# Optimization experiments

Hardware: AMD Instinct MI355X
Metric: run time of the kernel (lower is better)

## Reference

```python
import jax, jax.numpy as jnp
import numpy as np

B, S, D, H = 2, 2048, 1024, 16
DK = D // H  # 64

def setup_inputs() -> dict:
    key = jax.random.key(0)
    ks = jax.random.split(key, 12)
    scale = 1.0 / np.sqrt(D)
    return {
        "q": jax.random.normal(ks[0], (B, S, D), jnp.float32),
        "k": jax.random.normal(ks[1], (B, S, D), jnp.float32),
        "v": jax.random.normal(ks[2], (B, S, D), jnp.float32),
        "Wq": jax.random.normal(ks[3], (D, D), jnp.float32) * scale,
        "bq": jnp.zeros((D,), jnp.float32),
        "Wk": jax.random.normal(ks[4], (D, D), jnp.float32) * scale,
        "bk": jnp.zeros((D,), jnp.float32),
        "Wv": jax.random.normal(ks[5], (D, D), jnp.float32) * scale,
        "bv": jnp.zeros((D,), jnp.float32),
        "Wo": jax.random.normal(ks[6], (D, D), jnp.float32) * scale,
        "bo": jnp.zeros((D,), jnp.float32),
        "mask": jnp.ones((B, 1, S, S), jnp.bool_),
    }

def reference(q, k, v, Wq, bq, Wk, bk, Wv, bv, Wo, bo, mask):
    # Linear projections: y = x @ W^T + b (torch nn.Linear convention)
    def proj(x, W, b):
        return x @ W.T + b
    # [B,S,D] -> [B,H,S,DK]
    def split_heads(x):
        return x.reshape(B, S, H, DK).transpose(0, 2, 1, 3)

    query = split_heads(proj(q, Wq, bq))
    key_ = split_heads(proj(k, Wk, bk))
    value = split_heads(proj(v, Wv, bv))

    # NOTE: original uses out-of-place masked_fill whose result is discarded,
    # so mask has no effect on the computation (reproduced faithfully here).
    scores = jnp.einsum('bhqd,bhkd->bhqk', query, key_) / jnp.sqrt(
        jnp.asarray(DK, query.dtype))
    attn = jax.nn.softmax(scores, axis=-1)  # dropout p=0.0: identity
    x = jnp.einsum('bhqk,bhkd->bhqd', attn, value)
    x = x.transpose(0, 2, 1, 3).reshape(B, S, D)
    return proj(x, Wo, bo)
```

## Files before the change

kernel.cpp:

```cpp
#include <hip/hip_runtime.h>
#include <hip/hip_bf16.h>


typedef __attribute__((ext_vector_type(8))) short bf16x8;
typedef __attribute__((ext_vector_type(4))) float f32x4;
typedef unsigned short u16;
typedef unsigned int u32;

#define MFMA16(a, b, c) __builtin_amdgcn_mfma_f32_16x16x32_bf16(a, b, c, 0, 0, 0)
#define EXP2(x) __builtin_amdgcn_exp2f(x)

static __device__ __forceinline__ u16 f2bf(float f) {
    union { __hip_bfloat16 h; u16 u; } v;
    v.h = __float2bfloat16(f);
    return v.u;
}

static __device__ __forceinline__ u16 f2bf_fast(float f) {
    return (u16)((__float_as_uint(f) + 0x8000u) >> 16);
}

static __device__ __forceinline__ void gload16(const u16* g, u16* l) {
    __builtin_amdgcn_global_load_lds(
        (const __attribute__((address_space(1))) void*)g,
        (__attribute__((address_space(3))) void*)l, 16, 0, 0);
}

static __device__ __forceinline__ void cvt16(float4 f0, float4 f1,
                                             float4 f2, float4 f3, u16* o) {
    o[0]=f2bf(f0.x);  o[1]=f2bf(f0.y);  o[2]=f2bf(f0.z);  o[3]=f2bf(f0.w);
    o[4]=f2bf(f1.x);  o[5]=f2bf(f1.y);  o[6]=f2bf(f1.z);  o[7]=f2bf(f1.w);
    o[8]=f2bf(f2.x);  o[9]=f2bf(f2.y);  o[10]=f2bf(f2.z); o[11]=f2bf(f2.w);
    o[12]=f2bf(f3.x); o[13]=f2bf(f3.y); o[14]=f2bf(f3.z); o[15]=f2bf(f3.w);
}

#define CBARRIER()                                                             \
    do {                                                                       \
        asm volatile("s_waitcnt vmcnt(2) lgkmcnt(0)" ::: "memory");            \
        __builtin_amdgcn_sched_barrier(0);                                     \
        __builtin_amdgcn_s_barrier();                                          \
    } while (0)

struct CvtArgs16 { const float* in[16]; u16* out[16]; };

__global__ __launch_bounds__(256)
void cvt_multi(CvtArgs16 a)
{
    const int tsel = blockIdx.x >> 9;
    const int i = (((blockIdx.x & 511) * 256) + threadIdx.x) * 8;
    const float* in = a.in[tsel];
    u16* out = a.out[tsel];
    float4 x = *(const float4*)(in + i);
    float4 y = *(const float4*)(in + i + 4);
    u16 o[8];
    o[0]=f2bf(x.x); o[1]=f2bf(x.y); o[2]=f2bf(x.z); o[3]=f2bf(x.w);
    o[4]=f2bf(y.x); o[5]=f2bf(y.y); o[6]=f2bf(y.z); o[7]=f2bf(y.w);
    *(uint4*)(out + i) = *(uint4*)o;
}

struct GemmArgs {
    const float* F[3]; const u16* Wb[3]; const float* bias[3];
    u16* C[3]; float osc[3]; int epi[3];
};

__global__ __launch_bounds__(256)
void gemm_qkv(GemmArgs g)
{
    __shared__ u16 lds_f[2][128 * 32];
    __shared__ u16 lds_g[3][128 * 32];

    const int z = blockIdx.y;
    const float* Fp = g.F[z];
    const u16*  Gp = g.Wb[z];
    const int epi = g.epi[z];

    const int t    = threadIdx.x;
    const int lane = t & 63;
    const int w    = t >> 6;
    const int wm   = w >> 1, wn = w & 1;
    const int ll   = lane & 15;
    const int lg   = lane >> 4;

    const int bx  = blockIdx.x;
    const int swz = (bx & 7) * 32 + (bx >> 3);
    const int tile_m = (epi == 1 ? (swz & 7) : (swz >> 3)) * 128;
    const int tile_n = (epi == 1 ? (swz >> 3) : (swz & 7)) * 128;

    const int rowF = (epi == 1) ? tile_n : tile_m;
    const int rowG = (epi == 1) ? tile_m : tile_n;

    const int c0   = w * 2;
    const int lrow = lane >> 2;
    const int lcol = (lane & 3) * 8;

    const int srow = t >> 1;
    const int scol = (t & 1) * 16;
    const float* Fbase = Fp + (size_t)(rowF + srow) * 1024 + scol;
    const u16*   Gb0   = Gp + (size_t)(rowG + c0 * 16 + lrow) * 1024 + lcol;

    f32x4 acc[4][4] = {};
    float4 f0, f1, f2, f3;

    #define LOAD_F(s)                                                          \
    {                                                                          \
        const float* Fs = Fbase + (s) * 32;                                    \
        f0 = *(const float4*)(Fs);                                             \
        f1 = *(const float4*)(Fs + 4);                                         \
        f2 = *(const float4*)(Fs + 8);                                         \
        f3 = *(const float4*)(Fs + 12);                                        \
    }

    #define WRITE_F(buf)                                                       \
    {                                                                          \
        u16 tmp[16];                                                           \
        cvt16(f0, f1, f2, f3, tmp);                                            \
        *(uint4*)&lds_f[buf][srow * 32 + scol]     = *(uint4*)tmp;             \
        *(uint4*)&lds_f[buf][srow * 32 + scol + 8] = *(uint4*)(tmp + 8);       \
    }

    #define LOAD_G(buf, s)                                                     \
    {                                                                          \
        _Pragma("unroll")                                                      \
        for (int j = 0; j < 2; j++)                                            \
            gload16(Gb0 + (size_t)j * 16 * 1024 + (s) * 32,                    \
                    &lds_g[buf][(c0 + j) * 512]);                              \
    }

    #define DO_MFMA(gbuf, fbuf)                                                \
    {                                                                          \
        const u16* bA = (epi == 1) ? lds_g[gbuf] : lds_f[fbuf];                \
        const u16* bB = (epi == 1) ? lds_f[fbuf] : lds_g[gbuf];                \
        bf16x8 af[4], bfr[4];                                                  \
        _Pragma("unroll")                                                      \
        for (int i = 0; i < 4; i++)                                            \
            af[i] = *(bf16x8*)&bA[(wm * 64 + i * 16 + ll) * 32 + lg * 8];      \
        _Pragma("unroll")                                                      \
        for (int j = 0; j < 4; j++)                                            \
            bfr[j] = *(bf16x8*)&bB[(wn * 64 + j * 16 + ll) * 32 + lg * 8];     \
        _Pragma("unroll")                                                      \
        for (int i = 0; i < 4; i++)                                            \
            _Pragma("unroll")                                                  \
            for (int j = 0; j < 4; j++)                                        \
                acc[i][j] = MFMA16(af[i], bfr[j], acc[i][j]);                  \
    }

    LOAD_F(0);
    LOAD_G(0, 0);
    WRITE_F(0);
    LOAD_G(1, 1);
    CBARRIER();

    for (int s = 0; s < 32; ++s) {
        if (s + 1 < 32) LOAD_F(s + 1);
        if (s + 2 < 32) LOAD_G((s + 2) % 3, s + 2);
        DO_MFMA(s % 3, s & 1);
        if (s + 1 < 32) WRITE_F((s + 1) & 1);
        CBARRIER();
    }

    #undef LOAD_F
    #undef WRITE_F
    #undef LOAD_G
    #undef DO_MFMA

    const float osc = g.osc[z];
    const float* bias = g.bias[z];
    u16* Cp = g.C[z];

    #pragma unroll
    for (int i = 0; i < 4; i++) {
        const int row0 = tile_m + wm * 64 + i * 16 + lg * 4;
        #pragma unroll
        for (int j = 0; j < 4; j++) {
            const int col = tile_n + wn * 64 + j * 16 + ll;
            if (epi == 1) {
                const int b = col >> 11, s = col & 2047;
                #pragma unroll
                for (int r = 0; r < 4; r++)
                    Cp[(size_t)(b * 1024 + row0 + r) * 2048 + s] =
                        f2bf(acc[i][j][r] + bias[row0 + r]);
            } else {
                const float bias_v = bias[col];
                const int h = col >> 6, dk = col & 63;
                const int b = row0 >> 11;
                #pragma unroll
                for (int r = 0; r < 4; r++) {
                    const int s = (row0 + r) & 2047;
                    Cp[((size_t)(b * 16 + h) * 2048 + s) * 64 + dk] =
                        f2bf((acc[i][j][r] + bias_v) * osc);
                }
            }
        }
    }
}

__global__ __launch_bounds__(256)
void gemm_out(const u16* __restrict__ Ap, const u16* __restrict__ Wp,
              const float* __restrict__ bias, float* __restrict__ Cp)
{
    __shared__ u16 lds_a[2][128 * 32];
    __shared__ u16 lds_b[2][64 * 32];

    const int t    = threadIdx.x;
    const int lane = t & 63;
    const int w    = t >> 6;
    const int wm   = w >> 1, wn = w & 1;
    const int ll   = lane & 15;
    const int lg   = lane >> 4;

    const int bx  = blockIdx.x;
    const int swz = (bx & 7) * 64 + (bx >> 3);
    const int tile_m = (swz >> 4) * 128;
    const int tile_n = (swz & 15) * 64;

    const int lrow = lane >> 2;
    const int lcol = (lane & 3) * 8;

    f32x4 acc[4][2] = {};

    #define OSTAGE(buf, kt)                                                    \
    {                                                                          \
        _Pragma("unroll")                                                      \
        for (int j = 0; j < 3; j++) {                                          \
            const int c = w * 3 + j;                                           \
            if (c < 8) {                                                       \
                const int row = tile_m + c * 16 + lrow;                        \
                const int col = (kt) + lcol;                                   \
                const u16* ga = Ap + ((size_t)((row >> 11) * 16 + (col >> 6))  \
                                      * 2048 + (row & 2047)) * 64 + (col & 63);\
                gload16(ga, &lds_a[buf][c * 512]);                             \
            } else {                                                           \
                const int cc = c - 8;                                          \
                gload16(Wp + (size_t)(tile_n + cc * 16 + lrow) * 1024          \
                        + (kt) + lcol, &lds_b[buf][cc * 512]);                 \
            }                                                                  \
        }                                                                      \
    }

    OSTAGE(0, 0);
    __syncthreads();

    int cur = 0;
    for (int kt = 0; kt < 1024; kt += 32) {
        if (kt + 32 < 1024) OSTAGE(cur ^ 1, kt + 32);

        bf16x8 af[4], bfr[2];
        #pragma unroll
        for (int i = 0; i < 4; i++)
            af[i] = *(bf16x8*)&lds_a[cur][(wm * 64 + i * 16 + ll) * 32 + lg * 8];
        #pragma unroll
        for (int j = 0; j < 2; j++)
            bfr[j] = *(bf16x8*)&lds_b[cur][(wn * 32 + j * 16 + ll) * 32 + lg * 8];
        #pragma unroll
        for (int i = 0; i < 4; i++)
            #pragma unroll
            for (int j = 0; j < 2; j++)
                acc[i][j] = MFMA16(af[i], bfr[j], acc[i][j]);

        __syncthreads();
        cur ^= 1;
    }
    #undef OSTAGE

    #pragma unroll
    for (int i = 0; i < 4; i++) {
        const int row0 = tile_m + wm * 64 + i * 16 + lg * 4;
        #pragma unroll
        for (int j = 0; j < 2; j++) {
            const int col = tile_n + wn * 32 + j * 16 + ll;
            const float bias_v = bias[col];
            #pragma unroll
            for (int r = 0; r < 4; r++)
                Cp[(size_t)(row0 + r) * 1024 + col] = acc[i][j][r] + bias_v;
        }
    }
}

__global__ __launch_bounds__(512)
void attn_kernel(const u16* __restrict__ Qh, const u16* __restrict__ Kh,
                 const u16* __restrict__ Vt, u16* __restrict__ Oh)
{
    __shared__ u16 lds_k[2][64 * 64];
    __shared__ u16 lds_v[2][64 * 64];
    __shared__ u16 lds_p[8][16 * 64];

    const int t    = threadIdx.x;
    const int lane = t & 63;
    const int w    = t >> 6;
    const int ll   = lane & 15;
    const int lg   = lane >> 4;
    const int r7   = ll & 7;

    const int bx  = blockIdx.x;
    const int swz = (bx & 7) * 64 + (bx >> 3);
    const int qt = swz & 15;
    const int bh = swz >> 4;
    const int q0 = qt * 128 + w * 16;

    const u16* Qbase = Qh + ((size_t)bh * 2048 + q0 + ll) * 64 + lg * 8;
    const bf16x8 bq0 = *(const bf16x8*)(Qbase);
    const bf16x8 bq1 = *(const bf16x8*)(Qbase + 32);

    bf16x8 bones;
    #pragma unroll
    for (int i = 0; i < 8; i++) bones[i] = (short)0x3F80;

    f32x4 acc[4] = {};
    f32x4 acc_l = {};

    const int srow = lane >> 3;
    const int scol = 8 * ((lane & 7) ^ srow);
    const u16* Kg = Kh + (size_t)bh * 2048 * 64;
    const u16* Vg = Vt + (size_t)bh * 64 * 2048;

    #define ASTAGE(buf, kt)                                                    \
    {                                                                          \
        const int rr = w * 8 + srow;                                           \
        gload16(Kg + (size_t)((kt) + rr) * 64 + scol, &lds_k[buf][w * 512]);   \
        gload16(Vg + (size_t)rr * 2048 + (kt) + scol, &lds_v[buf][w * 512]);   \
    }

    ASTAGE(0, 0);
    __syncthreads();

    u16* lp = lds_p[w];
    int cur = 0;

    for (int kt = 0; kt < 2048; kt += 64) {
        if (kt + 64 < 2048) ASTAGE(cur ^ 1, kt + 64);

        f32x4 s[4];
        __builtin_amdgcn_s_setprio(1);
        #pragma unroll
        for (int ks = 0; ks < 4; ks++) {
            const u16* kp = &lds_k[cur][(ks * 16 + ll) * 64];
            const bf16x8 ak0 = *(const bf16x8*)(kp + ((lg * 8)      ^ (r7 * 8)));
            const bf16x8 ak1 = *(const bf16x8*)(kp + ((lg * 8 + 32) ^ (r7 * 8)));
            f32x4 z = {0.f, 0.f, 0.f, 0.f};
            z = MFMA16(ak0, bq0, z);
            z = MFMA16(ak1, bq1, z);
            s[ks] = z;
        }
        __builtin_amdgcn_s_setprio(0);

        #pragma unroll
        for (int ks = 0; ks < 4; ks++) {
            u16 pk[4];
            #pragma unroll
            for (int r = 0; r < 4; r++) pk[r] = f2bf_fast(EXP2(s[ks][r]));
            *(uint2*)&lp[ll * 64 + ((ks * 16 + lg * 4) ^ (r7 * 8))] = *(uint2*)pk;
        }

        __builtin_amdgcn_s_setprio(1);
        #pragma unroll
        for (int ks2 = 0; ks2 < 2; ks2++) {
            const int so = (ks2 * 32 + lg * 8) ^ (r7 * 8);
            const bf16x8 pa = *(const bf16x8*)&lp[ll * 64 + so];
            #pragma unroll
            for (int dt = 0; dt < 4; dt++) {
                const bf16x8 bv = *(const bf16x8*)&lds_v[cur][(dt * 16 + ll) * 64 + so];
                acc[dt] = MFMA16(pa, bv, acc[dt]);
            }
            acc_l = MFMA16(pa, bones, acc_l);
        }
        __builtin_amdgcn_s_setprio(0);

        __syncthreads();
        cur ^= 1;
    }
    #undef ASTAGE

    #pragma unroll
    for (int r = 0; r < 4; r++) {
        const float lq = 1.f / acc_l[r];
        const int qg = q0 + lg * 4 + r;
        u16* Op = Oh + ((size_t)bh * 2048 + qg) * 64 + ll;
        #pragma unroll
        for (int dt = 0; dt < 4; dt++)
            Op[dt * 16] = f2bf(acc[dt][r] * lq);
    }
}

extern "C" void kernel_launch(void* const* d_in, const int* in_sizes, int n_in,
                              void* d_out, int out_size, void* d_ws, size_t ws_size,
                              hipStream_t stream) {
    const float* q  = (const float*)d_in[0];
    const float* k  = (const float*)d_in[1];
    const float* v  = (const float*)d_in[2];
    const float* Wq = (const float*)d_in[3];
    const float* bq = (const float*)d_in[4];
    const float* Wk = (const float*)d_in[5];
    const float* bk = (const float*)d_in[6];
    const float* Wv = (const float*)d_in[7];
    const float* bv = (const float*)d_in[8];
    const float* Wo = (const float*)d_in[9];
    const float* bo = (const float*)d_in[10];
    float* out = (float*)d_out;

    const size_t M4 = (size_t)4 * 1024 * 1024;
    const size_t M1 = (size_t)1024 * 1024;
    const float qscale = 0.18033688011112042f;
    const dim3 blk(256);

    u16* Qh  = (u16*)d_ws;
    u16* Kh  = Qh + M4;
    u16* Vtb = Kh + M4;
    u16* Oh  = Vtb + M4;
    u16* Wqb = Oh + M4;
    u16* Wkb = Wqb + M1;
    u16* Wvb = Wkb + M1;
    u16* Wob = Wvb + M1;

    CvtArgs16 cv;
    for (int j = 0; j < 16; j++) { cv.in[j] = Wq; cv.out[j] = Wqb; }
    cv.in[0]=Wq; cv.out[0]=Wqb;
    cv.in[1]=Wk; cv.out[1]=Wkb;
    cv.in[2]=Wv; cv.out[2]=Wvb;
    cv.in[3]=Wo; cv.out[3]=Wob;
    cvt_multi<<<4 * 512, blk, 0, stream>>>(cv);

    GemmArgs ga;
    ga.F[0]=q;   ga.F[1]=k;   ga.F[2]=v;
    ga.Wb[0]=Wqb; ga.Wb[1]=Wkb; ga.Wb[2]=Wvb;
    ga.bias[0]=bq; ga.bias[1]=bk; ga.bias[2]=bv;
    ga.C[0]=Qh; ga.C[1]=Kh; ga.C[2]=Vtb;
    ga.osc[0]=qscale; ga.osc[1]=1.0f; ga.osc[2]=1.0f;
    ga.epi[0]=3; ga.epi[1]=3; ga.epi[2]=1;
    gemm_qkv<<<dim3(256, 3), blk, 0, stream>>>(ga);

    attn_kernel<<<512, dim3(512), 0, stream>>>(Qh, Kh, Vtb, Oh);

    gemm_out<<<512, blk, 0, stream>>>(Oh, Wob, bo, out);
}
```

Baseline: 123.7 us.

## Template QKV GEMM on epilogue, shrink weight tile to 64, double-buffer with syncthreads

```diff
diff --git a/kernel.cpp b/kernel.cpp
--- a/kernel.cpp
+++ b/kernel.cpp
@@ -33,13 +33,6 @@
     o[8]=f2bf(f2.x);  o[9]=f2bf(f2.y);  o[10]=f2bf(f2.z); o[11]=f2bf(f2.w);
     o[12]=f2bf(f3.x); o[13]=f2bf(f3.y); o[14]=f2bf(f3.z); o[15]=f2bf(f3.w);
 }
-
-#define CBARRIER()                                                             \
-    do {                                                                       \
-        asm volatile("s_waitcnt vmcnt(2) lgkmcnt(0)" ::: "memory");            \
-        __builtin_amdgcn_sched_barrier(0);                                     \
-        __builtin_amdgcn_s_barrier();                                          \
-    } while (0)
 
 struct CvtArgs16 { const float* in[16]; u16* out[16]; };
 
@@ -60,50 +53,56 @@
 
 struct GemmArgs {
     const float* F[3]; const u16* Wb[3]; const float* bias[3];
-    u16* C[3]; float osc[3]; int epi[3];
+    u16* C[3]; float osc[3];
 };
 
+template<int EPI>
 __global__ __launch_bounds__(256)
 void gemm_qkv(GemmArgs g)
 {
     __shared__ u16 lds_f[2][128 * 32];
-    __shared__ u16 lds_g[3][128 * 32];
-
-    const int z = blockIdx.y;
+    __shared__ u16 lds_g[2][64 * 32];
+
+    const int z = (EPI == 1) ? 2 : blockIdx.y;
     const float* Fp = g.F[z];
     const u16*  Gp = g.Wb[z];
-    const int epi = g.epi[z];
 
     const int t    = threadIdx.x;
     const int lane = t & 63;
     const int w    = t >> 6;
-    const int wm   = w >> 1, wn = w & 1;
     const int ll   = lane & 15;
     const int lg   = lane >> 4;
 
     const int bx  = blockIdx.x;
-    const int swz = (bx & 7) * 32 + (bx >> 3);
-    const int tile_m = (epi == 1 ? (swz & 7) : (swz >> 3)) * 128;
-    const int tile_n = (epi == 1 ? (swz >> 3) : (swz & 7)) * 128;
-
-    const int rowF = (epi == 1) ? tile_n : tile_m;
-    const int rowG = (epi == 1) ? tile_m : tile_n;
-
-    const int c0   = w * 2;
-    const int lrow = lane >> 2;
-    const int lcol = (lane & 3) * 8;
+    const int swz = (bx & 7) * 64 + (bx >> 3);
+    int tile_m, tile_n;
+    if (EPI == 1) { tile_m = (swz & 15) * 64;  tile_n = (swz >> 4) * 128; }
+    else          { tile_m = (swz >> 4) * 128; tile_n = (swz & 15) * 64;  }
+
+    const int rowF = (EPI == 1) ? tile_n : tile_m;
+    const int rowG = (EPI == 1) ? tile_m : tile_n;
+
+    const int wm = (EPI == 1) ? (w & 1) : (w >> 1);
+    const int wn = (EPI == 1) ? (w >> 1) : (w & 1);
+    constexpr int AI = (EPI == 1) ? 2 : 4;
+    constexpr int BJ = (EPI == 1) ? 4 : 2;
+    constexpr int MS = (EPI == 1) ? 32 : 64;
+    constexpr int NS = (EPI == 1) ? 64 : 32;
+
+    const int grow = lane >> 2;
+    const int gcol = (lane & 3) * 8;
+    const u16* Gb0 = Gp + (size_t)(rowG + w * 16 + grow) * 1024 + gcol;
 
     const int srow = t >> 1;
     const int scol = (t & 1) * 16;
     const float* Fbase = Fp + (size_t)(rowF + srow) * 1024 + scol;
-    const u16*   Gb0   = Gp + (size_t)(rowG + c0 * 16 + lrow) * 1024 + lcol;
-
-    f32x4 acc[4][4] = {};
+
+    f32x4 acc[AI][BJ] = {};
     float4 f0, f1, f2, f3;
 
     #define LOAD_F(s)                                                          \
     {                                                                          \
-        const float* Fs = Fbase + (s) * 32;                                    \
+        const float* Fs = Fbase + (s);                                         \
         f0 = *(const float4*)(Fs);                                             \
         f1 = *(const float4*)(Fs + 4);                                         \
         f2 = *(const float4*)(Fs + 8);                                         \
@@ -118,62 +117,61 @@
         *(uint4*)&lds_f[buf][srow * 32 + scol + 8] = *(uint4*)(tmp + 8);       \
     }
 
-    #define LOAD_G(buf, s)                                                     \
-    {                                                                          \
-        _Pragma("unroll")                                                      \
-        for (int j = 0; j < 2; j++)                                            \
-            gload16(Gb0 + (size_t)j * 16 * 1024 + (s) * 32,                    \
-                    &lds_g[buf][(c0 + j) * 512]);                              \
-    }
-
-    #define DO_MFMA(gbuf, fbuf)                                                \
-    {                                                                          \
-        const u16* bA = (epi == 1) ? lds_g[gbuf] : lds_f[fbuf];                \
-        const u16* bB = (epi == 1) ? lds_f[fbuf] : lds_g[gbuf];                \
-        bf16x8 af[4], bfr[4];                                                  \
-        _Pragma("unroll")                                                      \
-        for (int i = 0; i < 4; i++)                                            \
-            af[i] = *(bf16x8*)&bA[(wm * 64 + i * 16 + ll) * 32 + lg * 8];      \
-        _Pragma("unroll")                                                      \
-        for (int j = 0; j < 4; j++)                                            \
-            bfr[j] = *(bf16x8*)&bB[(wn * 64 + j * 16 + ll) * 32 + lg * 8];     \
-        _Pragma("unroll")                                                      \
-        for (int i = 0; i < 4; i++)                                            \
-            _Pragma("unroll")                                                  \
-            for (int j = 0; j < 4; j++)                                        \
-                acc[i][j] = MFMA16(af[i], bfr[j], acc[i][j]);                  \
-    }
-
+    gload16(Gb0, &lds_g[0][w * 512]);
     LOAD_F(0);
-    LOAD_G(0, 0);
     WRITE_F(0);
-    LOAD_G(1, 1);
-    CBARRIER();
-
-    for (int s = 0; s < 32; ++s) {
-        if (s + 1 < 32) LOAD_F(s + 1);
-        if (s + 2 < 32) LOAD_G((s + 2) % 3, s + 2);
-        DO_MFMA(s % 3, s & 1);
-        if (s + 1 < 32) WRITE_F((s + 1) & 1);
-        CBARRIER();
-    }
-
+    __syncthreads();
+
+    int cur = 0;
+    for (int kt = 0; kt < 1024; kt += 32) {
+        const int nxt = cur ^ 1;
+        const bool more = (kt + 32 < 1024);
+
+        if (more) {
+            LOAD_F(kt + 32);
+            gload16(Gb0 + kt + 32, &lds_g[nxt][w * 512]);
+        }
+
+        bf16x8 af[AI], bfr[BJ];
+        #pragma unroll
+        for (int i = 0; i < AI; i++) {
+            const int r = wm * MS + i * 16 + ll;
+            af[i] = (EPI == 1)
+                ? *(bf16x8*)&lds_g[cur][r * 32 + lg * 8]
+                : *(bf16x8*)&lds_f[cur][r * 32 + lg * 8];
+        }
+        #pragma unroll
+        for (int j = 0; j < BJ; j++) {
+            const int r = wn * NS + j * 16 + ll;
+            bfr[j] = (EPI == 1)
+                ? *(bf16x8*)&lds_f[cur][r * 32 + lg * 8]
+                : *(bf16x8*)&lds_g[cur][r * 32 + lg * 8];
+        }
+        #pragma unroll
+        for (int i = 0; i < AI; i++)
+            #pragma unroll
+            for (int j = 0; j < BJ; j++)
+                acc[i][j] = MFMA16(af[i], bfr[j], acc[i][j]);
+
+        if (more) WRITE_F(nxt);
+
+        __syncthreads();
+        cur = nxt;
+    }
     #undef LOAD_F
     #undef WRITE_F
-    #undef LOAD_G
-    #undef DO_MFMA
 
     const float osc = g.osc[z];
     const float* bias = g.bias[z];
     u16* Cp = g.C[z];
 
     #pragma unroll
-    for (int i = 0; i < 4; i++) {
-        const int row0 = tile_m + wm * 64 + i * 16 + lg * 4;
-        #pragma unroll
-        for (int j = 0; j < 4; j++) {
-            const int col = tile_n + wn * 64 + j * 16 + ll;
-            if (epi == 1) {
+    for (int i = 0; i < AI; i++) {
+        const int row0 = tile_m + wm * MS + i * 16 + lg * 4;
+        #pragma unroll
+        for (int j = 0; j < BJ; j++) {
+            const int col = tile_n + wn * NS + j * 16 + ll;
+            if (EPI == 1) {
                 const int b = col >> 11, s = col & 2047;
                 #pragma unroll
                 for (int r = 0; r < 4; r++)
@@ -425,8 +423,9 @@
     ga.bias[0]=bq; ga.bias[1]=bk; ga.bias[2]=bv;
     ga.C[0]=Qh; ga.C[1]=Kh; ga.C[2]=Vtb;
     ga.osc[0]=qscale; ga.osc[1]=1.0f; ga.osc[2]=1.0f;
-    ga.epi[0]=3; ga.epi[1]=3; ga.epi[2]=1;
-    gemm_qkv<<<dim3(256, 3), blk, 0, stream>>>(ga);
+
+    gemm_qkv<3><<<dim3(512, 2), blk, 0, stream>>>(ga);
+    gemm_qkv<1><<<dim3(512, 1), blk, 0, stream>>>(ga);
 
     attn_kernel<<<512, dim3(512), 0, stream>>>(Qh, Kh, Vtb, Oh);
 
```

After: 150.4 us. +21.6%, slower.
